# Kernel tuning notes

Hardware: AMD Instinct MI355X
Metric: run time of the kernel (lower is better)

The kernel has to match this reference:

```python
import jax, jax.numpy as jnp
import numpy as np

N_NODES = 10000
N_EDGES = 640000
D = 128
N_LAYERS = 4


def setup_inputs() -> dict:
    key = jax.random.key(0)
    k1, k2, k3, k4, k5 = jax.random.split(key, 5)
    node_feats = jax.random.normal(k1, (N_NODES, D), dtype=jnp.float32)
    src = jax.random.randint(k2, (N_EDGES,), 0, N_NODES, dtype=jnp.int32)
    dst = jax.random.randint(k3, (N_EDGES,), 0, N_NODES, dtype=jnp.int32)
    # stacked per-layer Linear params (all layers are 128 -> 128)
    Ws = jax.random.normal(k4, (N_LAYERS, D, D), dtype=jnp.float32) / np.sqrt(D).astype(np.float32)
    bs = jax.random.normal(k5, (N_LAYERS, D), dtype=jnp.float32) * 0.01
    return {"node_feats": node_feats, "src": src, "dst": dst, "Ws": Ws, "bs": bs}


def reference(node_feats, src, dst, Ws, bs):
    # Each GCN_layer: h = Linear(x); h = sum_{u in N(v)} h_u  (copy_u/sum)
    # dgl.add_self_loop => aggregate includes the node's own h, i.e. + h.
    # activation = relu; dropout is identity in eval; no batchnorm / residual.
    def step(h, params):
        W, b = params
        hl = h @ W + b                                   # [N, D] dense GEMM
        msgs = hl[src]                                   # [E, D] gather
        agg = jax.ops.segment_sum(msgs, dst, num_segments=N_NODES) + hl  # scatter-sum + self-loop
        return jax.nn.relu(agg), None

    h, _ = jax.lax.scan(step, node_feats, (Ws, bs))
    return h
```

## Files before the change

### kernel.cpp

```cpp
#include <hip/hip_runtime.h>
#include <hip/hip_bf16.h>

#define N_NODES 10000
#define N_EDGES 640000
#define D 128
#define N_LAYERS 4

#define NBINS 79
#define BIN_CAP 10240
#define WT_LD 136
#define POISON 0xAAAAAAAAu

typedef unsigned uv4 __attribute__((ext_vector_type(4)));
typedef short bf16x8 __attribute__((ext_vector_type(8)));
typedef float f32x4 __attribute__((ext_vector_type(4)));
typedef float f32x2 __attribute__((ext_vector_type(2)));


__global__ __launch_bounds__(256) void binA_kernel(const int* __restrict__ src,
                                                   const int* __restrict__ dst,
                                                   unsigned* __restrict__ binCursor,
                                                   unsigned* __restrict__ binbuf) {
    __shared__ int cnt[NBINS];
    __shared__ int gbase[NBINS];
    const int t = threadIdx.x;
    if (t < NBINS) cnt[t] = 0;
    __syncthreads();

    const int e0 = blockIdx.x * 2560;
    unsigned key[10];
    int bin[10], pos[10];
#pragma unroll
    for (int j = 0; j < 10; ++j) {
        int e = e0 + j * 256 + t;
        int d = dst[e];
        int s = src[e];
        key[j] = ((unsigned)d << 14) | (unsigned)s;
        bin[j] = d >> 7;
        pos[j] = atomicAdd(&cnt[bin[j]], 1);
    }
    __syncthreads();
    if (t < NBINS) {
        unsigned old = atomicAdd(&binCursor[t], (unsigned)cnt[t]);
        gbase[t] = (int)(old - POISON);
    }
    __syncthreads();
#pragma unroll
    for (int j = 0; j < 10; ++j) {
        int p = gbase[bin[j]] + pos[j];
        if (p >= 0 && p < BIN_CAP) binbuf[bin[j] * BIN_CAP + p] = key[j];
    }
}

__global__ __launch_bounds__(256) void binB_kernel(unsigned* __restrict__ binbuf,
                                                   const unsigned* __restrict__ binCursor,
                                                   int* __restrict__ begs,
                                                   int* __restrict__ degs) {
    __shared__ unsigned buf[BIN_CAP];
    __shared__ int deg[128], base[128], cur[128];
    const int b = blockIdx.x;
    const int t = threadIdx.x;
    int m = (int)(binCursor[b] - POISON);
    if (m > BIN_CAP) m = BIN_CAP;
    if (m < 0) m = 0;

    if (t < 128) deg[t] = 0;
    __syncthreads();

    for (int i = t; i < m; i += 256) {
        unsigned k = binbuf[(size_t)b * BIN_CAP + i];
        buf[i] = k;
        atomicAdd(&deg[(k >> 14) & 127], 1);
    }
    __syncthreads();

    if (t < 64) {
        int a0 = deg[2 * t], a1 = deg[2 * t + 1];
        int s = a0 + a1;
        int x = s;
#pragma unroll
        for (int off = 1; off < 64; off <<= 1) {
            int tt = __shfl_up(x, off);
            if (t >= off) x += tt;
        }
        base[2 * t]     = x - s;
        base[2 * t + 1] = x - a1;
        cur[2 * t]      = x - s;
        cur[2 * t + 1]  = x - a1;
    }
    __syncthreads();

    if (t < 128) {
        int v = b * 128 + t;
        if (v < N_NODES) {
            degs[v] = deg[t];
            begs[v] = b * BIN_CAP + base[t];
        }
    }

    for (int i = t; i < m; i += 256) {
        unsigned k = buf[i];
        int p = atomicAdd(&cur[(k >> 14) & 127], 1);
        binbuf[(size_t)b * BIN_CAP + p] = k & 0x3FFFu;
    }
}


template<bool FP32IN>
__global__ __launch_bounds__(512) void gemm_mfma(const void* __restrict__ hv,
                                                 const float* __restrict__ W,
                                                 const float* __restrict__ bias,
                                                 unsigned short* __restrict__ hl) {
    __shared__ __hip_bfloat16 Wt[128 * WT_LD];
    __shared__ float bs_s[D];
    const int t = threadIdx.x;

    for (int i = t; i < D * D; i += 512) {
        int k = i >> 7, n = i & 127;
        Wt[n * WT_LD + k] = __float2bfloat16(W[i]);
    }
    if (t < D) bs_s[t] = bias[t];
    __syncthreads();

    const int wave = t >> 6;
    const int lane = t & 63;
    const int ln = lane & 15;
    const int q = lane >> 4;
    const int row0 = blockIdx.x * 128 + wave * 16;

    int m = row0 + ln;
    if (m > N_NODES - 1) m = N_NODES - 1;

    f32x4 acc[8];
#pragma unroll
    for (int n0 = 0; n0 < 8; ++n0) acc[n0] = (f32x4){0.f, 0.f, 0.f, 0.f};

#pragma unroll
    for (int k0 = 0; k0 < 128; k0 += 32) {
        bf16x8 a;
        if (FP32IN) {
            const float* hf = (const float*)hv;
            float4 f0 = *(const float4*)(hf + (size_t)m * D + k0 + q * 8);
            float4 f1 = *(const float4*)(hf + (size_t)m * D + k0 + q * 8 + 4);
            union { bf16x8 v; __hip_bfloat16 b[8]; } pk;
            pk.b[0] = __float2bfloat16(f0.x); pk.b[1] = __float2bfloat16(f0.y);
            pk.b[2] = __float2bfloat16(f0.z); pk.b[3] = __float2bfloat16(f0.w);
            pk.b[4] = __float2bfloat16(f1.x); pk.b[5] = __float2bfloat16(f1.y);
            pk.b[6] = __float2bfloat16(f1.z); pk.b[7] = __float2bfloat16(f1.w);
            a = pk.v;
        } else {
            const unsigned short* hb = (const unsigned short*)hv;
            a = *(const bf16x8*)(hb + (size_t)m * D + k0 + q * 8);
        }
#pragma unroll
        for (int n0 = 0; n0 < 8; ++n0) {
            bf16x8 b = *(const bf16x8*)(&Wt[(n0 * 16 + ln) * WT_LD + k0 + q * 8]);
            acc[n0] = __builtin_amdgcn_mfma_f32_16x16x32_bf16(a, b, acc[n0], 0, 0, 0);
        }
    }

#pragma unroll
    for (int n0 = 0; n0 < 8; ++n0) {
        float bv = bs_s[n0 * 16 + ln];
#pragma unroll
        for (int r = 0; r < 4; ++r) {
            int row = row0 + q * 4 + r;
            if (row < N_NODES) {
                __hip_bfloat16 o = __float2bfloat16(acc[n0][r] + bv);
                hl[(size_t)row * D + n0 * 16 + ln] = *(unsigned short*)&o;
            }
        }
    }
}


__device__ __forceinline__ float bf_lo(unsigned u) {
    u <<= 16; return __builtin_bit_cast(float, u);
}
__device__ __forceinline__ float bf_hi(unsigned u) {
    u &= 0xffff0000u; return __builtin_bit_cast(float, u);
}
__device__ __forceinline__ f32x2 bf_pair(unsigned u) {
    return (f32x2){bf_lo(u), bf_hi(u)};
}

template<bool FINAL>
__global__ __launch_bounds__(256) void aggregate_kernel(const uv4* __restrict__ hlq,
                                                        const int* __restrict__ begs,
                                                        const int* __restrict__ degs,
                                                        const int* __restrict__ csr,
                                                        float* __restrict__ outf,
                                                        unsigned short* __restrict__ outb) {
    int node = blockIdx.x * 4 + (threadIdx.x >> 6);
    if (node >= N_NODES) return;
    const int lane = threadIdx.x & 63;
    const int g = lane >> 4;
    const int c = lane & 15;

    const int beg = begs[node];
    const int end = beg + degs[node];

    f32x2 a0 = (f32x2){0.f, 0.f}, a1 = a0, a2 = a0, a3 = a0;
    if (g == 0) {
        uv4 s = hlq[node * 16 + c];
        a0 = bf_pair(s.x); a1 = bf_pair(s.y);
        a2 = bf_pair(s.z); a3 = bf_pair(s.w);
    }

    for (int eb = beg; eb < end; eb += 64) {
        int ce = eb + lane;
        int cv = csr[ce < end ? ce : (end - 1)];
#pragma unroll
        for (int half = 0; half < 2; ++half) {
            int b0 = eb + 32 * half;
            if (b0 < end) {
#pragma unroll
                for (int j = 0; j < 8; ++j) {
                    int e0 = b0 + 4 * j;
                    if (e0 < end) {
                        int e = e0 + g;
                        int u = __shfl(cv, 32 * half + 4 * j + g);
                        uv4 v = hlq[u * 16 + c];
                        if (e >= end) { v.x = 0u; v.y = 0u; v.z = 0u; v.w = 0u; }
                        a0 += bf_pair(v.x);
                        a1 += bf_pair(v.y);
                        a2 += bf_pair(v.z);
                        a3 += bf_pair(v.w);
                    }
                }
            }
        }
    }

#pragma unroll
    for (int off = 16; off <= 32; off <<= 1) {
        a0.x += __shfl_xor(a0.x, off); a0.y += __shfl_xor(a0.y, off);
        a1.x += __shfl_xor(a1.x, off); a1.y += __shfl_xor(a1.y, off);
        a2.x += __shfl_xor(a2.x, off); a2.y += __shfl_xor(a2.y, off);
        a3.x += __shfl_xor(a3.x, off); a3.y += __shfl_xor(a3.y, off);
    }

    if (g == 0) {
        if (FINAL) {
            float4 o0, o1;
            o0.x = fmaxf(a0.x, 0.f); o0.y = fmaxf(a0.y, 0.f);
            o0.z = fmaxf(a1.x, 0.f); o0.w = fmaxf(a1.y, 0.f);
            o1.x = fmaxf(a2.x, 0.f); o1.y = fmaxf(a2.y, 0.f);
            o1.z = fmaxf(a3.x, 0.f); o1.w = fmaxf(a3.y, 0.f);
            float4* orow = (float4*)(outf + (size_t)node * D);
            orow[c * 2]     = o0;
            orow[c * 2 + 1] = o1;
        } else {
            union { uint4 u; __hip_bfloat16 b[8]; } o;
            o.b[0] = __float2bfloat16(fmaxf(a0.x, 0.f));
            o.b[1] = __float2bfloat16(fmaxf(a0.y, 0.f));
            o.b[2] = __float2bfloat16(fmaxf(a1.x, 0.f));
            o.b[3] = __float2bfloat16(fmaxf(a1.y, 0.f));
            o.b[4] = __float2bfloat16(fmaxf(a2.x, 0.f));
            o.b[5] = __float2bfloat16(fmaxf(a2.y, 0.f));
            o.b[6] = __float2bfloat16(fmaxf(a3.x, 0.f));
            o.b[7] = __float2bfloat16(fmaxf(a3.y, 0.f));
            *(uint4*)(outb + (size_t)node * D + c * 8) = o.u;
        }
    }
}


extern "C" void kernel_launch(void* const* d_in, const int* in_sizes, int n_in,
                              void* d_out, int out_size, void* d_ws, size_t ws_size,
                              hipStream_t stream) {
    const float* node_feats = (const float*)d_in[0];
    const int*   src        = (const int*)d_in[1];
    const int*   dst        = (const int*)d_in[2];
    const float* Ws         = (const float*)d_in[3];
    const float* bs         = (const float*)d_in[4];
    float* out = (float*)d_out;

    char* ws = (char*)d_ws;
    unsigned* binCursor     = (unsigned*)(ws + 0);
    int*      begs          = (int*)(ws + 1024);
    int*      degs          = (int*)(ws + 41984);
    unsigned* binbuf        = (unsigned*)(ws + 82944);
    unsigned short* hl      = (unsigned short*)(ws + 3318784);
    unsigned short* hagg    = (unsigned short*)(ws + 5878784);

    binA_kernel<<<250, 256, 0, stream>>>(src, dst, binCursor, binbuf);
    binB_kernel<<<NBINS, 256, 0, stream>>>(binbuf, binCursor, begs, degs);

    const void* hin = (const void*)node_feats;
    for (int l = 0; l < N_LAYERS; ++l) {
        if (l == 0) {
            gemm_mfma<true><<<(N_NODES + 127) / 128, 512, 0, stream>>>(
                hin, Ws + (size_t)l * D * D, bs + (size_t)l * D, hl);
        } else {
            gemm_mfma<false><<<(N_NODES + 127) / 128, 512, 0, stream>>>(
                hin, Ws + (size_t)l * D * D, bs + (size_t)l * D, hl);
        }
        if (l < N_LAYERS - 1) {
            aggregate_kernel<false><<<(N_NODES + 3) / 4, 256, 0, stream>>>(
                (const uv4*)hl, begs, degs, (const int*)binbuf, nullptr, hagg);
            hin = (const void*)hagg;
        } else {
            aggregate_kernel<true><<<(N_NODES + 3) / 4, 256, 0, stream>>>(
                (const uv4*)hl, begs, degs, (const int*)binbuf, out, nullptr);
        }
    }
}
```

Before: 181.2 us.

## Fuse aggregation with next-layer GEMM and pretranspose weights once in binning kernel

```diff
diff --git a/kernel.cpp b/kernel.cpp
--- a/kernel.cpp
+++ b/kernel.cpp
@@ -8,8 +8,8 @@
 
 #define NBINS 79
 #define BIN_CAP 10240
-#define WT_LD 136
 #define POISON 0xAAAAAAAAu
+#define A_LD 136
 
 typedef unsigned uv4 __attribute__((ext_vector_type(4)));
 typedef short bf16x8 __attribute__((ext_vector_type(8)));
@@ -17,17 +17,36 @@
 typedef float f32x2 __attribute__((ext_vector_type(2)));
 
 
-__global__ __launch_bounds__(256) void binA_kernel(const int* __restrict__ src,
-                                                   const int* __restrict__ dst,
-                                                   unsigned* __restrict__ binCursor,
-                                                   unsigned* __restrict__ binbuf) {
+__global__ __launch_bounds__(256) void binA_wt_kernel(const int* __restrict__ src,
+                                                      const int* __restrict__ dst,
+                                                      unsigned* __restrict__ binCursor,
+                                                      unsigned* __restrict__ binbuf,
+                                                      const float* __restrict__ W,
+                                                      unsigned short* __restrict__ Wt) {
     __shared__ int cnt[NBINS];
     __shared__ int gbase[NBINS];
     const int t = threadIdx.x;
+    const int b = blockIdx.x;
+
+    if (b >= 250) {
+        const int g = (b - 250) * 256 + t;
+        const int e0 = g * 8;
+        const int l = e0 >> 14;
+        const int r = e0 & 16383;
+        const int n = r >> 7;
+        const int k0 = r & 127;
+        union { bf16x8 v; __hip_bfloat16 h[8]; } pk;
+#pragma unroll
+        for (int j = 0; j < 8; ++j)
+            pk.h[j] = __float2bfloat16(W[l * 16384 + (k0 + j) * 128 + n]);
+        *(bf16x8*)(Wt + e0) = pk.v;
+        return;
+    }
+
     if (t < NBINS) cnt[t] = 0;
     __syncthreads();
 
-    const int e0 = blockIdx.x * 2560;
+    const int e0 = b * 2560;
     unsigned key[10];
     int bin[10], pos[10];
 #pragma unroll
@@ -106,27 +125,16 @@
 }
 
 
-template<bool FP32IN>
-__global__ __launch_bounds__(512) void gemm_mfma(const void* __restrict__ hv,
-                                                 const float* __restrict__ W,
-                                                 const float* __restrict__ bias,
-                                                 unsigned short* __restrict__ hl) {
-    __shared__ __hip_bfloat16 Wt[128 * WT_LD];
-    __shared__ float bs_s[D];
+__global__ __launch_bounds__(256) void gemm0_kernel(const float* __restrict__ hf,
+                                                    const unsigned short* __restrict__ WtL,
+                                                    const float* __restrict__ bias,
+                                                    unsigned short* __restrict__ hl) {
     const int t = threadIdx.x;
-
-    for (int i = t; i < D * D; i += 512) {
-        int k = i >> 7, n = i & 127;
-        Wt[n * WT_LD + k] = __float2bfloat16(W[i]);
-    }
-    if (t < D) bs_s[t] = bias[t];
-    __syncthreads();
-
     const int wave = t >> 6;
     const int lane = t & 63;
     const int ln = lane & 15;
     const int q = lane >> 4;
-    const int row0 = blockIdx.x * 128 + wave * 16;
+    const int row0 = blockIdx.x * 64 + wave * 16;
 
     int m = row0 + ln;
     if (m > N_NODES - 1) m = N_NODES - 1;
@@ -137,31 +145,24 @@
 
 #pragma unroll
     for (int k0 = 0; k0 < 128; k0 += 32) {
-        bf16x8 a;
-        if (FP32IN) {
-            const float* hf = (const float*)hv;
-            float4 f0 = *(const float4*)(hf + (size_t)m * D + k0 + q * 8);
-            float4 f1 = *(const float4*)(hf + (size_t)m * D + k0 + q * 8 + 4);
-            union { bf16x8 v; __hip_bfloat16 b[8]; } pk;
-            pk.b[0] = __float2bfloat16(f0.x); pk.b[1] = __float2bfloat16(f0.y);
-            pk.b[2] = __float2bfloat16(f0.z); pk.b[3] = __float2bfloat16(f0.w);
-            pk.b[4] = __float2bfloat16(f1.x); pk.b[5] = __float2bfloat16(f1.y);
-            pk.b[6] = __float2bfloat16(f1.z); pk.b[7] = __float2bfloat16(f1.w);
-            a = pk.v;
-        } else {
-            const unsigned short* hb = (const unsigned short*)hv;
-            a = *(const bf16x8*)(hb + (size_t)m * D + k0 + q * 8);
-        }
+        float4 f0 = *(const float4*)(hf + (size_t)m * D + k0 + q * 8);
+        float4 f1 = *(const float4*)(hf + (size_t)m * D + k0 + q * 8 + 4);
+        union { bf16x8 v; __hip_bfloat16 b[8]; } pk;
+        pk.b[0] = __float2bfloat16(f0.x); pk.b[1] = __float2bfloat16(f0.y);
+        pk.b[2] = __float2bfloat16(f0.z); pk.b[3] = __float2bfloat16(f0.w);
+        pk.b[4] = __float2bfloat16(f1.x); pk.b[5] = __float2bfloat16(f1.y);
+        pk.b[6] = __float2bfloat16(f1.z); pk.b[7] = __float2bfloat16(f1.w);
+        bf16x8 a = pk.v;
 #pragma unroll
         for (int n0 = 0; n0 < 8; ++n0) {
-            bf16x8 b = *(const bf16x8*)(&Wt[(n0 * 16 + ln) * WT_LD + k0 + q * 8]);
-            acc[n0] = __builtin_amdgcn_mfma_f32_16x16x32_bf16(a, b, acc[n0], 0, 0, 0);
+            bf16x8 bb = *(const bf16x8*)(WtL + (size_t)(n0 * 16 + ln) * D + k0 + q * 8);
+            acc[n0] = __builtin_amdgcn_mfma_f32_16x16x32_bf16(a, bb, acc[n0], 0, 0, 0);
         }
     }
 
 #pragma unroll
     for (int n0 = 0; n0 < 8; ++n0) {
-        float bv = bs_s[n0 * 16 + ln];
+        float bv = bias[n0 * 16 + ln];
 #pragma unroll
         for (int r = 0; r < 4; ++r) {
             int row = row0 + q * 4 + r;
@@ -173,7 +174,6 @@
     }
 }
 
-
 __device__ __forceinline__ float bf_lo(unsigned u) {
     u <<= 16; return __builtin_bit_cast(float, u);
 }
@@ -184,15 +184,11 @@
     return (f32x2){bf_lo(u), bf_hi(u)};
 }
 
-template<bool FINAL>
-__global__ __launch_bounds__(256) void aggregate_kernel(const uv4* __restrict__ hlq,
-                                                        const int* __restrict__ begs,
-                                                        const int* __restrict__ degs,
-                                                        const int* __restrict__ csr,
-                                                        float* __restrict__ outf,
-                                                        unsigned short* __restrict__ outb) {
-    int node = blockIdx.x * 4 + (threadIdx.x >> 6);
-    if (node >= N_NODES) return;
+__device__ __forceinline__ void agg_rows(int node, const uv4* __restrict__ hlq,
+                                         const int* __restrict__ begs,
+                                         const int* __restrict__ degs,
+                                         const int* __restrict__ csr,
+                                         f32x2& a0, f32x2& a1, f32x2& a2, f32x2& a3) {
     const int lane = threadIdx.x & 63;
     const int g = lane >> 4;
     const int c = lane & 15;
@@ -200,11 +196,11 @@
     const int beg = begs[node];
     const int end = beg + degs[node];
 
-    f32x2 a0 = (f32x2){0.f, 0.f}, a1 = a0, a2 = a0, a3 = a0;
+    a0 = (f32x2){0.f, 0.f}; a1 = a0; a2 = a0; a3 = a0;
     if (g == 0) {
-        uv4 s = hlq[node * 16 + c];
-        a0 = bf_pair(s.x); a1 = bf_pair(s.y);
-        a2 = bf_pair(s.z); a3 = bf_pair(s.w);
+        uv4 sv = hlq[node * 16 + c];
+        a0 = bf_pair(sv.x); a1 = bf_pair(sv.y);
+        a2 = bf_pair(sv.z); a3 = bf_pair(sv.w);
     }
 
     for (int eb = beg; eb < end; eb += 64) {
@@ -239,29 +235,81 @@
         a2.x += __shfl_xor(a2.x, off); a2.y += __shfl_xor(a2.y, off);
         a3.x += __shfl_xor(a3.x, off); a3.y += __shfl_xor(a3.y, off);
     }
+}
+
+__global__ __launch_bounds__(1024, 8) void agg_gemm_kernel(
+        const uv4* __restrict__ hlq, const int* __restrict__ begs,
+        const int* __restrict__ degs, const int* __restrict__ csr,
+        const unsigned short* __restrict__ WtL, const float* __restrict__ bias,
+        unsigned short* __restrict__ hlo) {
+    __shared__ __hip_bfloat16 Arow[16 * A_LD];
+    const int t = threadIdx.x;
+    const int wave = t >> 6;
+    const int lane = t & 63;
+    const int g = lane >> 4;
+    const int c = lane & 15;
+    const int node = blockIdx.x * 16 + wave;
+
+    f32x2 a0, a1, a2, a3;
+    agg_rows(node, hlq, begs, degs, csr, a0, a1, a2, a3);
 
     if (g == 0) {
-        if (FINAL) {
-            float4 o0, o1;
-            o0.x = fmaxf(a0.x, 0.f); o0.y = fmaxf(a0.y, 0.f);
-            o0.z = fmaxf(a1.x, 0.f); o0.w = fmaxf(a1.y, 0.f);
-            o1.x = fmaxf(a2.x, 0.f); o1.y = fmaxf(a2.y, 0.f);
-            o1.z = fmaxf(a3.x, 0.f); o1.w = fmaxf(a3.y, 0.f);
-            float4* orow = (float4*)(outf + (size_t)node * D);
-            orow[c * 2]     = o0;
-            orow[c * 2 + 1] = o1;
-        } else {
-            union { uint4 u; __hip_bfloat16 b[8]; } o;
-            o.b[0] = __float2bfloat16(fmaxf(a0.x, 0.f));
-            o.b[1] = __float2bfloat16(fmaxf(a0.y, 0.f));
-            o.b[2] = __float2bfloat16(fmaxf(a1.x, 0.f));
-            o.b[3] = __float2bfloat16(fmaxf(a1.y, 0.f));
-            o.b[4] = __float2bfloat16(fmaxf(a2.x, 0.f));
-            o.b[5] = __float2bfloat16(fmaxf(a2.y, 0.f));
-            o.b[6] = __float2bfloat16(fmaxf(a3.x, 0.f));
-            o.b[7] = __float2bfloat16(fmaxf(a3.y, 0.f));
-            *(uint4*)(outb + (size_t)node * D + c * 8) = o.u;
-        }
+        union { bf16x8 v; __hip_bfloat16 h[8]; } pk;
+        pk.h[0] = __float2bfloat16(fmaxf(a0.x, 0.f));
+        pk.h[1] = __float2bfloat16(fmaxf(a0.y, 0.f));
+        pk.h[2] = __float2bfloat16(fmaxf(a1.x, 0.f));
+        pk.h[3] = __float2bfloat16(fmaxf(a1.y, 0.f));
+        pk.h[4] = __float2bfloat16(fmaxf(a2.x, 0.f));
+        pk.h[5] = __float2bfloat16(fmaxf(a2.y, 0.f));
+        pk.h[6] = __float2bfloat16(fmaxf(a3.x, 0.f));
+        pk.h[7] = __float2bfloat16(fmaxf(a3.y, 0.f));
+        *(bf16x8*)&Arow[wave * A_LD + c * 8] = pk.v;
+    }
+    __syncthreads();
+
+    if (wave < 8) {
+        const int ln = lane & 15;
+        const int q = lane >> 4;
+        f32x4 acc = (f32x4){0.f, 0.f, 0.f, 0.f};
+#pragma unroll
+        for (int k0 = 0; k0 < 128; k0 += 32) {
+            bf16x8 a = *(const bf16x8*)&Arow[ln * A_LD + k0 + q * 8];
+            bf16x8 bb = *(const bf16x8*)(WtL + (size_t)(wave * 16 + ln) * D + k0 + q * 8);
+            acc = __builtin_amdgcn_mfma_f32_16x16x32_bf16(a, bb, acc, 0, 0, 0);
+        }
+        float bv = bias[wave * 16 + ln];
+#pragma unroll
+        for (int r = 0; r < 4; ++r) {
+            int row = blockIdx.x * 16 + q * 4 + r;
+            __hip_bfloat16 o = __float2bfloat16(acc[r] + bv);
+            hlo[(size_t)row * D + wave * 16 + ln] = *(unsigned short*)&o;
+        }
+    }
+}
+
+__global__ __launch_bounds__(256) void agg_final_kernel(const uv4* __restrict__ hlq,
+                                                        const int* __restrict__ begs,
+                                                        const int* __restrict__ degs,
+                                                        const int* __restrict__ csr,
+                                                        float* __restrict__ outf) {
+    int node = blockIdx.x * 4 + (threadIdx.x >> 6);
+    if (node >= N_NODES) return;
+    const int lane = threadIdx.x & 63;
+    const int g = lane >> 4;
+    const int c = lane & 15;
+
+    f32x2 a0, a1, a2, a3;
+    agg_rows(node, hlq, begs, degs, csr, a0, a1, a2, a3);
+
+    if (g == 0) {
+        float4 o0, o1;
+        o0.x = fmaxf(a0.x, 0.f); o0.y = fmaxf(a0.y, 0.f);
+        o0.z = fmaxf(a1.x, 0.f); o0.w = fmaxf(a1.y, 0.f);
+        o1.x = fmaxf(a2.x, 0.f); o1.y = fmaxf(a2.y, 0.f);
+        o1.z = fmaxf(a3.x, 0.f); o1.w = fmaxf(a3.y, 0.f);
+        float4* orow = (float4*)(outf + (size_t)node * D);
+        orow[c * 2]     = o0;
+        orow[c * 2 + 1] = o1;
     }
 }
 
@@ -281,28 +329,20 @@
     int*      begs          = (int*)(ws + 1024);
     int*      degs          = (int*)(ws + 41984);
     unsigned* binbuf        = (unsigned*)(ws + 82944);
-    unsigned short* hl      = (unsigned short*)(ws + 3318784);
-    unsigned short* hagg    = (unsigned short*)(ws + 5878784);
-
-    binA_kernel<<<250, 256, 0, stream>>>(src, dst, binCursor, binbuf);
+    unsigned short* hlA     = (unsigned short*)(ws + 3318784);
+    unsigned short* hlB     = (unsigned short*)(ws + 5878784);
+    unsigned short* Wt      = (unsigned short*)(ws + 8438784);
+    const int* csr = (const int*)binbuf;
+
+    binA_wt_kernel<<<282, 256, 0, stream>>>(src, dst, binCursor, binbuf, Ws, Wt);
     binB_kernel<<<NBINS, 256, 0, stream>>>(binbuf, binCursor, begs, degs);
 
-    const void* hin = (const void*)node_feats;
-    for (int l = 0; l < N_LAYERS; ++l) {
-        if (l == 0) {
-            gemm_mfma<true><<<(N_NODES + 127) / 128, 512, 0, stream>>>(
-                hin, Ws + (size_t)l * D * D, bs + (size_t)l * D, hl);
-        } else {
-            gemm_mfma<false><<<(N_NODES + 127) / 128, 512, 0, stream>>>(
-                hin, Ws + (size_t)l * D * D, bs + (size_t)l * D, hl);
-        }
-        if (l < N_LAYERS - 1) {
-            aggregate_kernel<false><<<(N_NODES + 3) / 4, 256, 0, stream>>>(
-                (const uv4*)hl, begs, degs, (const int*)binbuf, nullptr, hagg);
-            hin = (const void*)hagg;
-        } else {
-            aggregate_kernel<true><<<(N_NODES + 3) / 4, 256, 0, stream>>>(
-                (const uv4*)hl, begs, degs, (const int*)binbuf, out, nullptr);
-        }
-    }
-}
+    gemm0_kernel<<<157, 256, 0, stream>>>(node_feats, Wt, bs, hlA);
+    agg_gemm_kernel<<<625, 1024, 0, stream>>>((const uv4*)hlA, begs, degs, csr,
+                                              Wt + 1 * 16384, bs + 1 * D, hlB);
+    agg_gemm_kernel<<<625, 1024, 0, stream>>>((const uv4*)hlB, begs, degs, csr,
+                                              Wt + 2 * 16384, bs + 2 * D, hlA);
+    agg_gemm_kernel<<<625, 1024, 0, stream>>>((const uv4*)hlA, begs, degs, csr,
+                                              Wt + 3 * 16384, bs + 3 * D, hlB);
+    agg_final_kernel<<<2500, 256, 0, stream>>>((const uv4*)hlB, begs, degs, csr, out);
+}
```

Result: faster. 173.6 us (-4.2%).
